# Optimization experiments

Measured on AMD Instinct MI355X. Metric: run time of the kernel, lower is better.

## Reference

```python
import jax, jax.numpy as jnp
import numpy as np

NEG_INF = -9e15
ALPHA = 0.2  # LeakyReLU negative slope


def setup_inputs() -> dict:
    key = jax.random.key(0)
    k1, k2, k3, k4 = jax.random.split(key, 4)
    B, N, C_IN, C_OUT, H = 8, 2048, 256, 256, 4
    node_feats = jax.random.normal(k1, (B, N, C_IN), dtype=jnp.float32)
    adj_matrix = jax.random.randint(k2, (B, N, N), 0, 2, dtype=jnp.int32)
    # include self-connections as the docstring expects
    eye = jnp.eye(N, dtype=jnp.int32)[None]
    adj_matrix = jnp.maximum(adj_matrix, eye)
    W = jax.random.normal(k3, (C_OUT, C_IN), dtype=jnp.float32) * (1.414 / np.sqrt(C_IN))
    b = jnp.zeros((C_OUT,), dtype=jnp.float32)
    a = jax.random.normal(k4, (H, 2 * (C_OUT // H)), dtype=jnp.float32) * 0.1
    return {"node_feats": node_feats, "adj_matrix": adj_matrix, "W": W, "b": b, "a": a}


def reference(node_feats, adj_matrix, W, b, a):
    B, N, _ = node_feats.shape
    H, two_c = a.shape
    c = two_c // 2
    # projection: [B, N, H, c]
    f = (jnp.einsum('bni,oi->bno', node_feats, W) + b).reshape(B, N, H, c)
    # attention logit for edge (i, j): leakyrelu(a . [f_i, f_j])
    # decomposes as leakyrelu(s_src[i] + s_dst[j])
    a_src, a_dst = a[:, :c], a[:, c:]
    s_src = jnp.einsum('bnhc,hc->bnh', f, a_src)  # [B, N, H]
    s_dst = jnp.einsum('bnhc,hc->bnh', f, a_dst)  # [B, N, H]
    logits = jax.nn.leaky_relu(s_src[:, :, None, :] + s_dst[:, None, :, :], ALPHA)  # [B,N,N,H]
    logits = jnp.where(adj_matrix[..., None] == 1, logits, NEG_INF)
    probs = jax.nn.softmax(logits, axis=2)  # softmax over source nodes j
    out = jnp.einsum('bijh,bjhc->bihc', probs, f)
    return out.reshape(B, N, H * c)  # concat_heads=True
```

## Files before the change

### kernel.cpp

```cpp
#include <hip/hip_runtime.h>

#define LOG2E 1.4426950408889634f

typedef __attribute__((ext_vector_type(8))) short bf16x8;
typedef __attribute__((ext_vector_type(4))) float f32x4;

union AF { unsigned u[4]; bf16x8 v; };

__device__ __forceinline__ unsigned short f2bf(float f) {
  unsigned int u = __float_as_uint(f);
  u = (u + 0x7fffu + ((u >> 16) & 1u)) >> 16;
  return (unsigned short)u;
}

__global__ __launch_bounds__(256) void gat_k1(
    const float* __restrict__ X, const float* __restrict__ W,
    const float* __restrict__ bias, const float* __restrict__ a,
    unsigned short* __restrict__ ft, float* __restrict__ ssrc,
    float* __restrict__ sdst)
{
  __shared__ float Xs[8][128];
  __shared__ float Ws[8][128];
  const int tid = threadIdx.x;
  const int tx = tid & 15, ty = tid >> 4;
  const int m0 = blockIdx.x * 128;
  const int c0 = blockIdx.y * 128;

  float acc[8][8];
#pragma unroll
  for (int r = 0; r < 8; ++r)
#pragma unroll
    for (int j = 0; j < 8; ++j) acc[r][j] = 0.f;

  const int lrow = tid >> 1;
  const int kk0 = (tid & 1) * 4;
  const float* Xp = X + (size_t)(m0 + lrow) * 256 + kk0;
  const float* Wp = W + (size_t)(c0 + lrow) * 256 + kk0;

  for (int kc = 0; kc < 256; kc += 8) {
    float4 xv = *(const float4*)(Xp + kc);
    float4 wv = *(const float4*)(Wp + kc);
    __syncthreads();
    Xs[kk0 + 0][lrow] = xv.x; Xs[kk0 + 1][lrow] = xv.y;
    Xs[kk0 + 2][lrow] = xv.z; Xs[kk0 + 3][lrow] = xv.w;
    Ws[kk0 + 0][lrow] = wv.x; Ws[kk0 + 1][lrow] = wv.y;
    Ws[kk0 + 2][lrow] = wv.z; Ws[kk0 + 3][lrow] = wv.w;
    __syncthreads();
#pragma unroll
    for (int kk = 0; kk < 8; ++kk) {
      float av[8], wv8[8];
#pragma unroll
      for (int r = 0; r < 8; ++r) av[r] = Xs[kk][ty * 8 + r];
#pragma unroll
      for (int j = 0; j < 8; ++j) wv8[j] = Ws[kk][tx * 8 + j];
#pragma unroll
      for (int r = 0; r < 8; ++r)
#pragma unroll
        for (int j = 0; j < 8; ++j) acc[r][j] = fmaf(av[r], wv8[j], acc[r][j]);
    }
  }

  const int b = m0 >> 11;
  const int nloc0 = (m0 & 2047) + ty * 8;
  const int cg0 = c0 + tx * 8;
  const int h = cg0 >> 6;
  const int cb = cg0 & 63;

  float bv[8], av_s[8], av_d[8];
#pragma unroll
  for (int j = 0; j < 8; ++j) {
    bv[j]   = bias[cg0 + j];
    av_s[j] = a[h * 128 + cb + j];
    av_d[j] = a[h * 128 + 64 + cb + j];
  }
#pragma unroll
  for (int r = 0; r < 8; ++r)
#pragma unroll
    for (int j = 0; j < 8; ++j) acc[r][j] += bv[j];

  const int jt = nloc0 >> 4;
  const int ni = nloc0 & 15;
#pragma unroll
  for (int j = 0; j < 8; ++j) {
    unsigned int u[4];
#pragma unroll
    for (int q = 0; q < 4; ++q) {
      unsigned int lo = f2bf(acc[2 * q + 0][j]);
      unsigned int hi = f2bf(acc[2 * q + 1][j]);
      u[q] = lo | (hi << 16);
    }
    size_t off = ((((size_t)b * 128 + jt) * 4 + h) * 64 + (cb + j)) * 16 + ni;
    *(uint4*)(ft + off) = make_uint4(u[0], u[1], u[2], u[3]);
  }

  float sp[8], dp[8];
#pragma unroll
  for (int r = 0; r < 8; ++r) {
    float s = 0.f, d = 0.f;
#pragma unroll
    for (int j = 0; j < 8; ++j) {
      s = fmaf(acc[r][j], av_s[j], s);
      d = fmaf(acc[r][j], av_d[j], d);
    }
    sp[r] = s; dp[r] = d;
  }
#pragma unroll
  for (int off = 1; off < 8; off <<= 1) {
#pragma unroll
    for (int r = 0; r < 8; ++r) {
      sp[r] += __shfl_xor(sp[r], off);
      dp[r] += __shfl_xor(dp[r], off);
    }
  }
  if ((tx & 7) == 0) {
    float* sb = ssrc + ((size_t)b * 4 + h) * 2048 + nloc0;
    float* db = sdst + ((size_t)b * 4 + h) * 2048 + nloc0;
#pragma unroll
    for (int r = 0; r < 8; ++r) { sb[r] = sp[r] * LOG2E; db[r] = dp[r] * LOG2E; }
  }
}

__global__ __launch_bounds__(512, 6) void gat_k2(
    const int* __restrict__ adj, const unsigned short* __restrict__ ft,
    const float* __restrict__ ssrc, const float* __restrict__ sdst,
    float* __restrict__ out)
{
  __shared__ __align__(16) unsigned char lds[37120];
  float* sd = (float*)lds;
  unsigned* Aw = (unsigned*)(lds + 32768);

  const int tid = threadIdx.x;
  const int b = blockIdx.x & 7;
  const int itile = blockIdx.x >> 3;
  const int i0 = itile * 16;
  const int w = tid >> 6;
  const int h = w >> 1;
  const int p = w & 1;
  const int lane = tid & 63;
  const int i_l = lane & 15;
  const int kg = lane >> 4;
  const int shamt = kg * 8;

  const bf16x8* fp = (const bf16x8*)ft +
      ((((size_t)b * 128 + p * 64 + (kg >> 1)) * 4 + h) * 64 + i_l) * 2 +
      (kg & 1);

  bf16x8 A0 = fp[0], A1 = fp[32], A2 = fp[64], A3 = fp[96];
  fp += 1024;
  bf16x8 B0 = fp[0], B1 = fp[32], B2 = fp[64], B3 = fp[96];
  fp += 1024;

  {
    const float4* src = (const float4*)(sdst + (size_t)b * 4 * 2048);
    float4* dst = (float4*)sd;
#pragma unroll
    for (int q = 0; q < 4; ++q) dst[tid + q * 512] = src[tid + q * 512];
  }
  {
    const int* abase = adj + (size_t)b * 2048 * 2048 + (size_t)i0 * 2048;
    unsigned short* dst16 = (unsigned short*)Aw;
#pragma unroll
    for (int k = 0; k < 4; ++k) {
      const int idx = k * 512 + tid;
      const int r = idx >> 7;
      const int s16 = idx & 127;
      const int4* ap = (const int4*)(abase + (size_t)r * 2048 + s16 * 16);
      int4 v0 = ap[0], v1 = ap[1], v2 = ap[2], v3 = ap[3];
      int vv[16] = {v0.x, v0.y, v0.z, v0.w, v1.x, v1.y, v1.z, v1.w,
                    v2.x, v2.y, v2.z, v2.w, v3.x, v3.y, v3.z, v3.w};
      unsigned m = 0;
#pragma unroll
      for (int i = 0; i < 16; ++i) m |= (vv[i] ? 1u : 0u) << i;
      dst16[((s16 >> 1) * 17 + r) * 2 + (s16 & 1)] = (unsigned short)m;
    }
  }
  const float si = ssrc[((size_t)b * 4 + h) * 2048 + i0 + i_l];

  const unsigned* awp = Aw + (p * 32) * 17 + i_l;
  const float* sdp = sd + h * 2048 + p * 1024 + kg * 8;

  f32x4 acc0, acc1, acc2, acc3, acc4;
#pragma unroll
  for (int q = 0; q < 4; ++q) {
    acc0[q] = 0.f; acc1[q] = 0.f; acc2[q] = 0.f; acc3[q] = 0.f; acc4[q] = 0.f;
  }
  bf16x8 ones;
#pragma unroll
  for (int q = 0; q < 8; ++q) ones[q] = (short)0x3F80;

  __syncthreads();

#define STEP(mw_, t0_, t1_, F0_, F1_, F2_, F3_)                    \
  {                                                                \
    const unsigned byte_ = ((mw_) >> shamt) & 0xffu;               \
    float tj_[8] = {t0_.x, t0_.y, t0_.z, t0_.w,                    \
                    t1_.x, t1_.y, t1_.z, t1_.w};                   \
    float e_[8];                                                   \
    _Pragma("unroll")                                              \
    for (int q = 0; q < 8; ++q) {                                  \
      float x_ = si + tj_[q];                                      \
      float y_ = fmaxf(x_, 0.2f * x_);                             \
      float ev_ = __builtin_amdgcn_exp2f(y_);                      \
      e_[q] = (byte_ & (1u << q)) ? ev_ : 0.f;                     \
    }                                                              \
    AF af_;                                                        \
    _Pragma("unroll")                                              \
    for (int q2 = 0; q2 < 4; ++q2) {                               \
      unsigned r_;                                                 \
      asm("v_cvt_pk_bf16_f32 %0, %1, %2"                           \
          : "=v"(r_) : "v"(e_[2 * q2]), "v"(e_[2 * q2 + 1]));      \
      af_.u[q2] = r_;                                              \
    }                                                              \
    acc0 = __builtin_amdgcn_mfma_f32_16x16x32_bf16(af_.v, F0_, acc0, 0, 0, 0); \
    acc1 = __builtin_amdgcn_mfma_f32_16x16x32_bf16(af_.v, F1_, acc1, 0, 0, 0); \
    acc2 = __builtin_amdgcn_mfma_f32_16x16x32_bf16(af_.v, F2_, acc2, 0, 0, 0); \
    acc3 = __builtin_amdgcn_mfma_f32_16x16x32_bf16(af_.v, F3_, acc3, 0, 0, 0); \
    acc4 = __builtin_amdgcn_mfma_f32_16x16x32_bf16(af_.v, ones, acc4, 0, 0, 0); \
  }

  unsigned mwA, mwB;
  float4 ta0, ta1, tb0, tb1;
  mwA = awp[0];
  ta0 = *(const float4*)sdp;
  ta1 = *(const float4*)(sdp + 4);
  awp += 17; sdp += 32;

  for (int s = 0; s < 30; s += 2) {
    mwB = awp[0];
    tb0 = *(const float4*)sdp;
    tb1 = *(const float4*)(sdp + 4);
    awp += 17; sdp += 32;
    STEP(mwA, ta0, ta1, A0, A1, A2, A3)
    A0 = fp[0]; A1 = fp[32]; A2 = fp[64]; A3 = fp[96];
    fp += 1024;
    mwA = awp[0];
    ta0 = *(const float4*)sdp;
    ta1 = *(const float4*)(sdp + 4);
    awp += 17; sdp += 32;
    STEP(mwB, tb0, tb1, B0, B1, B2, B3)
    B0 = fp[0]; B1 = fp[32]; B2 = fp[64]; B3 = fp[96];
    fp += 1024;
  }
  mwB = awp[0];
  tb0 = *(const float4*)sdp;
  tb1 = *(const float4*)(sdp + 4);
  STEP(mwA, ta0, ta1, A0, A1, A2, A3)
  STEP(mwB, tb0, tb1, B0, B1, B2, B3)
#undef STEP

  float* ep = (float*)lds;
  float* el = (float*)(lds + 16384);
  __syncthreads();
  if (p == 1) {
#pragma unroll
    for (int r = 0; r < 4; ++r) {
      const int row = kg * 4 + r;
      ep[(h * 16 + row) * 64 + 0  + i_l] = acc0[r];
      ep[(h * 16 + row) * 64 + 16 + i_l] = acc1[r];
      ep[(h * 16 + row) * 64 + 32 + i_l] = acc2[r];
      ep[(h * 16 + row) * 64 + 48 + i_l] = acc3[r];
    }
    if (i_l == 0) {
#pragma unroll
      for (int r = 0; r < 4; ++r) el[h * 16 + kg * 4 + r] = acc4[r];
    }
  }
  __syncthreads();
  if (p == 0) {
    float* ob = out + ((size_t)(b * 2048 + i0)) * 256 + h * 64;
#pragma unroll
    for (int r = 0; r < 4; ++r) {
      const int row = kg * 4 + r;
      const float L = acc4[r] + el[h * 16 + row];
      const float ri = 1.0f / L;
      ob[(size_t)row * 256 + 0  + i_l] = (acc0[r] + ep[(h * 16 + row) * 64 + 0  + i_l]) * ri;
      ob[(size_t)row * 256 + 16 + i_l] = (acc1[r] + ep[(h * 16 + row) * 64 + 16 + i_l]) * ri;
      ob[(size_t)row * 256 + 32 + i_l] = (acc2[r] + ep[(h * 16 + row) * 64 + 32 + i_l]) * ri;
      ob[(size_t)row * 256 + 48 + i_l] = (acc3[r] + ep[(h * 16 + row) * 64 + 48 + i_l]) * ri;
    }
  }
}

extern "C" void kernel_launch(void* const* d_in, const int* in_sizes, int n_in,
                              void* d_out, int out_size, void* d_ws, size_t ws_size,
                              hipStream_t stream) {
  const float* X    = (const float*)d_in[0];
  const int*   adj  = (const int*)d_in[1];
  const float* W    = (const float*)d_in[2];
  const float* bias = (const float*)d_in[3];
  const float* a    = (const float*)d_in[4];
  float* out = (float*)d_out;

  unsigned short* ft = (unsigned short*)d_ws;
  float* ssrc = (float*)((char*)d_ws + 8388608);
  float* sdst = ssrc + 8 * 4 * 2048;

  gat_k1<<<dim3(128, 2, 1), 256, 0, stream>>>(X, W, bias, a, ft, ssrc, sdst);
  gat_k2<<<dim3(1024, 1, 1), 512, 0, stream>>>(adj, ft, ssrc, sdst, out);
}
```

Measured before the change: 104.6 us.

## Tile 64 rows per block with streamed double-buffered adjacency mask

The attention kernel now handles 64 query rows per 1024-thread block instead of 16 rows per 512-thread block. Each wave covers its own 16-row group over the full source range, so the cross-wave partial-sum reduction through LDS goes away. The adjacency bitmask is streamed in 256-column windows with a double-buffered LDS pack overlapped with compute, and each block loads sdst once for four times as many rows. The cost is a __syncthreads per window, only 256 blocks in the grid, and no split of the j range within a block, which may limit parallelism.

```diff
diff --git a/kernel.cpp b/kernel.cpp
--- a/kernel.cpp
+++ b/kernel.cpp
@@ -120,64 +120,70 @@
   }
 }
 
-__global__ __launch_bounds__(512, 6) void gat_k2(
+__global__ __launch_bounds__(1024, 4) void gat_k2(
     const int* __restrict__ adj, const unsigned short* __restrict__ ft,
     const float* __restrict__ ssrc, const float* __restrict__ sdst,
     float* __restrict__ out)
 {
-  __shared__ __align__(16) unsigned char lds[37120];
+  __shared__ __align__(16) unsigned char lds[36928];
   float* sd = (float*)lds;
-  unsigned* Aw = (unsigned*)(lds + 32768);
+  unsigned* Awin = (unsigned*)(lds + 32768);
 
   const int tid = threadIdx.x;
   const int b = blockIdx.x & 7;
   const int itile = blockIdx.x >> 3;
-  const int i0 = itile * 16;
-  const int w = tid >> 6;
-  const int h = w >> 1;
-  const int p = w & 1;
+  const int i0 = itile * 64;
+  const int wv = tid >> 6;
+  const int h = wv >> 2;
+  const int rg = wv & 3;
   const int lane = tid & 63;
   const int i_l = lane & 15;
   const int kg = lane >> 4;
   const int shamt = kg * 8;
 
   const bf16x8* fp = (const bf16x8*)ft +
-      ((((size_t)b * 128 + p * 64 + (kg >> 1)) * 4 + h) * 64 + i_l) * 2 +
-      (kg & 1);
-
-  bf16x8 A0 = fp[0], A1 = fp[32], A2 = fp[64], A3 = fp[96];
-  fp += 1024;
-  bf16x8 B0 = fp[0], B1 = fp[32], B2 = fp[64], B3 = fp[96];
-  fp += 1024;
+      ((((size_t)b * 128 + (kg >> 1)) * 4 + h) * 64 + i_l) * 2 + (kg & 1);
+
+  bf16x8 A0, A1, A2, A3, B0, B1, B2, B3;
+#define LDF(F0_, F1_, F2_, F3_)                                    \
+  { F0_ = fp[0]; F1_ = fp[32]; F2_ = fp[64]; F3_ = fp[96]; fp += 1024; }
+
+  LDF(A0, A1, A2, A3)
+  LDF(B0, B1, B2, B3)
 
   {
     const float4* src = (const float4*)(sdst + (size_t)b * 4 * 2048);
     float4* dst = (float4*)sd;
-#pragma unroll
-    for (int q = 0; q < 4; ++q) dst[tid + q * 512] = src[tid + q * 512];
-  }
+    dst[tid]        = src[tid];
+    dst[tid + 1024] = src[tid + 1024];
+  }
+
+  const int arow = tid >> 4;
+  const int ajg  = tid & 15;
+  const int* abase = adj + (size_t)b * 4194304 +
+                     (size_t)(i0 + arow) * 2048 + ajg * 16;
+
+#define PACKW(bufbit, v0_, v1_, v2_, v3_)                          \
+  {                                                                \
+    int vv[16] = {v0_.x, v0_.y, v0_.z, v0_.w, v1_.x, v1_.y,        \
+                  v1_.z, v1_.w, v2_.x, v2_.y, v2_.z, v2_.w,        \
+                  v3_.x, v3_.y, v3_.z, v3_.w};                     \
+    unsigned m_ = 0;                                               \
+    _Pragma("unroll")                                              \
+    for (int i = 0; i < 16; ++i) m_ |= (vv[i] ? 1u : 0u) << i;     \
+    ((unsigned short*)Awin)[(((bufbit) * 8 + (ajg >> 1)) * 65 +    \
+                             arow) * 2 + (ajg & 1)] = (unsigned short)m_; \
+  }
+
   {
-    const int* abase = adj + (size_t)b * 2048 * 2048 + (size_t)i0 * 2048;
-    unsigned short* dst16 = (unsigned short*)Aw;
-#pragma unroll
-    for (int k = 0; k < 4; ++k) {
-      const int idx = k * 512 + tid;
-      const int r = idx >> 7;
-      const int s16 = idx & 127;
-      const int4* ap = (const int4*)(abase + (size_t)r * 2048 + s16 * 16);
-      int4 v0 = ap[0], v1 = ap[1], v2 = ap[2], v3 = ap[3];
-      int vv[16] = {v0.x, v0.y, v0.z, v0.w, v1.x, v1.y, v1.z, v1.w,
-                    v2.x, v2.y, v2.z, v2.w, v3.x, v3.y, v3.z, v3.w};
-      unsigned m = 0;
-#pragma unroll
-      for (int i = 0; i < 16; ++i) m |= (vv[i] ? 1u : 0u) << i;
-      dst16[((s16 >> 1) * 17 + r) * 2 + (s16 & 1)] = (unsigned short)m;
-    }
-  }
-  const float si = ssrc[((size_t)b * 4 + h) * 2048 + i0 + i_l];
-
-  const unsigned* awp = Aw + (p * 32) * 17 + i_l;
-  const float* sdp = sd + h * 2048 + p * 1024 + kg * 8;
+    const int4* ap = (const int4*)abase;
+    int4 q0 = ap[0], q1 = ap[1], q2 = ap[2], q3 = ap[3];
+    PACKW(0, q0, q1, q2, q3)
+  }
+
+  const float si = ssrc[((size_t)b * 4 + h) * 2048 + i0 + rg * 16 + i_l];
+  const float* sdp = sd + h * 2048 + kg * 8;
+  const unsigned* aw0 = Awin + rg * 16 + i_l;
 
   f32x4 acc0, acc1, acc2, acc3, acc4;
 #pragma unroll
@@ -190,9 +196,12 @@
 
   __syncthreads();
 
-#define STEP(mw_, t0_, t1_, F0_, F1_, F2_, F3_)                    \
+#define STEPX(jj_, F0_, F1_, F2_, F3_)                             \
   {                                                                \
-    const unsigned byte_ = ((mw_) >> shamt) & 0xffu;               \
+    const unsigned mw_ = awb[(jj_) * 65];                          \
+    float4 t0_ = *(const float4*)(sdp + (jj_) * 32);               \
+    float4 t1_ = *(const float4*)(sdp + (jj_) * 32 + 4);           \
+    const unsigned byte_ = (mw_ >> shamt) & 0xffu;                 \
     float tj_[8] = {t0_.x, t0_.y, t0_.z, t0_.w,                    \
                     t1_.x, t1_.y, t1_.z, t1_.w};                   \
     float e_[8];                                                   \
@@ -218,66 +227,38 @@
     acc4 = __builtin_amdgcn_mfma_f32_16x16x32_bf16(af_.v, ones, acc4, 0, 0, 0); \
   }
 
-  unsigned mwA, mwB;
-  float4 ta0, ta1, tb0, tb1;
-  mwA = awp[0];
-  ta0 = *(const float4*)sdp;
-  ta1 = *(const float4*)(sdp + 4);
-  awp += 17; sdp += 32;
-
-  for (int s = 0; s < 30; s += 2) {
-    mwB = awp[0];
-    tb0 = *(const float4*)sdp;
-    tb1 = *(const float4*)(sdp + 4);
-    awp += 17; sdp += 32;
-    STEP(mwA, ta0, ta1, A0, A1, A2, A3)
-    A0 = fp[0]; A1 = fp[32]; A2 = fp[64]; A3 = fp[96];
-    fp += 1024;
-    mwA = awp[0];
-    ta0 = *(const float4*)sdp;
-    ta1 = *(const float4*)(sdp + 4);
-    awp += 17; sdp += 32;
-    STEP(mwB, tb0, tb1, B0, B1, B2, B3)
-    B0 = fp[0]; B1 = fp[32]; B2 = fp[64]; B3 = fp[96];
-    fp += 1024;
-  }
-  mwB = awp[0];
-  tb0 = *(const float4*)sdp;
-  tb1 = *(const float4*)(sdp + 4);
-  STEP(mwA, ta0, ta1, A0, A1, A2, A3)
-  STEP(mwB, tb0, tb1, B0, B1, B2, B3)
-#undef STEP
-
-  float* ep = (float*)lds;
-  float* el = (float*)(lds + 16384);
-  __syncthreads();
-  if (p == 1) {
-#pragma unroll
-    for (int r = 0; r < 4; ++r) {
-      const int row = kg * 4 + r;
-      ep[(h * 16 + row) * 64 + 0  + i_l] = acc0[r];
-      ep[(h * 16 + row) * 64 + 16 + i_l] = acc1[r];
-      ep[(h * 16 + row) * 64 + 32 + i_l] = acc2[r];
-      ep[(h * 16 + row) * 64 + 48 + i_l] = acc3[r];
-    }
-    if (i_l == 0) {
-#pragma unroll
-      for (int r = 0; r < 4; ++r) el[h * 16 + kg * 4 + r] = acc4[r];
-    }
-  }
-  __syncthreads();
-  if (p == 0) {
-    float* ob = out + ((size_t)(b * 2048 + i0)) * 256 + h * 64;
-#pragma unroll
-    for (int r = 0; r < 4; ++r) {
-      const int row = kg * 4 + r;
-      const float L = acc4[r] + el[h * 16 + row];
-      const float ri = 1.0f / L;
-      ob[(size_t)row * 256 + 0  + i_l] = (acc0[r] + ep[(h * 16 + row) * 64 + 0  + i_l]) * ri;
-      ob[(size_t)row * 256 + 16 + i_l] = (acc1[r] + ep[(h * 16 + row) * 64 + 16 + i_l]) * ri;
-      ob[(size_t)row * 256 + 32 + i_l] = (acc2[r] + ep[(h * 16 + row) * 64 + 32 + i_l]) * ri;
-      ob[(size_t)row * 256 + 48 + i_l] = (acc3[r] + ep[(h * 16 + row) * 64 + 48 + i_l]) * ri;
-    }
+  for (int w = 0; w < 8; ++w) {
+    int4 v0, v1, v2, v3;
+    if (w < 7) {
+      const int4* ap = (const int4*)(abase + (w + 1) * 256);
+      v0 = ap[0]; v1 = ap[1]; v2 = ap[2]; v3 = ap[3];
+    }
+    const unsigned* awb = aw0 + (w & 1) * 520;
+    STEPX(0, A0, A1, A2, A3) LDF(A0, A1, A2, A3)
+    STEPX(1, B0, B1, B2, B3) LDF(B0, B1, B2, B3)
+    STEPX(2, A0, A1, A2, A3) LDF(A0, A1, A2, A3)
+    STEPX(3, B0, B1, B2, B3) LDF(B0, B1, B2, B3)
+    STEPX(4, A0, A1, A2, A3) LDF(A0, A1, A2, A3)
+    STEPX(5, B0, B1, B2, B3) LDF(B0, B1, B2, B3)
+    STEPX(6, A0, A1, A2, A3) LDF(A0, A1, A2, A3)
+    STEPX(7, B0, B1, B2, B3) LDF(B0, B1, B2, B3)
+    sdp += 256;
+    if (w < 7) PACKW((w + 1) & 1, v0, v1, v2, v3)
+    __syncthreads();
+  }
+#undef STEPX
+#undef LDF
+#undef PACKW
+
+  float* ob = out + ((size_t)(b * 2048 + i0 + rg * 16)) * 256 + h * 64;
+#pragma unroll
+  for (int r = 0; r < 4; ++r) {
+    const int row = kg * 4 + r;
+    const float ri = 1.0f / acc4[r];
+    ob[(size_t)row * 256 + 0  + i_l] = acc0[r] * ri;
+    ob[(size_t)row * 256 + 16 + i_l] = acc1[r] * ri;
+    ob[(size_t)row * 256 + 32 + i_l] = acc2[r] * ri;
+    ob[(size_t)row * 256 + 48 + i_l] = acc3[r] * ri;
   }
 }
 
@@ -296,5 +277,5 @@
   float* sdst = ssrc + 8 * 4 * 2048;
 
   gat_k1<<<dim3(128, 2, 1), 256, 0, stream>>>(X, W, bias, a, ft, ssrc, sdst);
-  gat_k2<<<dim3(1024, 1, 1), 512, 0, stream>>>(adj, ft, ssrc, sdst, out);
-}
+  gat_k2<<<dim3(256, 1, 1), 1024, 0, stream>>>(adj, ft, ssrc, sdst, out);
+}
```

Result: slower. 113.5 us (+8.4%).
